# Optimization experiments

Measured on AMD Instinct MI355X. Metric: run time of the kernel, lower is better.

The kernel has to match this reference:

```python
import jax, jax.numpy as jnp
import numpy as np

N_ATOMS = 500_000
N_PAIRS = 16_000_000
A0 = 0.5291772105638411
KE = 14.399645351950548
KEHALF = KE / 2.0


def softplus_inverse(x):
    # inverse of softplus: log(exp(x) - 1)
    return float(np.log(np.expm1(x)))


def setup_inputs() -> dict:
    key = jax.random.key(0)
    k_z, k_r, k_c, k_i, k_j = jax.random.split(key, 5)
    Zf = jax.random.randint(k_z, (N_ATOMS,), 1, 95).astype(jnp.float32)
    rij = jax.random.uniform(k_r, (N_PAIRS,), minval=0.5, maxval=5.0, dtype=jnp.float32)
    cutoff_values = jax.random.uniform(k_c, (N_PAIRS,), dtype=jnp.float32)
    idx_i = jax.random.randint(k_i, (N_PAIRS,), 0, N_ATOMS)
    idx_j = jax.random.randint(k_j, (N_PAIRS,), 0, N_ATOMS)
    p = lambda v: jnp.full((1,), softplus_inverse(v), dtype=jnp.float32)
    return {
        "N": N_ATOMS,
        "Zf": Zf,
        "rij": rij,
        "cutoff_values": cutoff_values,
        "idx_i": idx_i,
        "idx_j": idx_j,
        "adiv": p(1.0 / (0.8854 * A0)),
        "apow": p(0.23),
        "c1": p(0.1818),
        "c2": p(0.5099),
        "c3": p(0.2802),
        "c4": p(0.02817),
        "a1": p(3.2),
        "a2": p(0.9423),
        "a3": p(0.4028),
        "a4": p(0.2016),
    }


def reference(N, Zf, rij, cutoff_values, idx_i, idx_j,
              adiv, apow, c1, c2, c3, c4, a1, a2, a3, a4):
    sp = jax.nn.softplus
    # per-atom screened charge: [N]
    z = Zf ** sp(apow)
    # per-pair screening length: [P]
    a = (z[idx_i] + z[idx_j]) * sp(adiv)
    a1p = sp(a1) * a
    a2p = sp(a2) * a
    a3p = sp(a3) * a
    a4p = sp(a4) * a
    c1p, c2p, c3p, c4p = sp(c1), sp(c2), sp(c3), sp(c4)
    csum = c1p + c2p + c3p + c4p
    c1n, c2n, c3n, c4n = c1p / csum, c2p / csum, c3p / csum, c4p / csum
    zizj = Zf[idx_i] * Zf[idx_j]
    f = (c1n * jnp.exp(-a1p * rij)
         + c2n * jnp.exp(-a2p * rij)
         + c3n * jnp.exp(-a3p * rij)
         + c4n * jnp.exp(-a4p * rij)) * cutoff_values
    contrib = KEHALF * f * zizj / rij  # [P]
    return jnp.zeros((N,), dtype=Zf.dtype).at[idx_i].add(contrib)
```

## Files before the change

kernel.cpp:

```cpp
#include <hip/hip_runtime.h>
#include <hip/hip_fp16.h>

static constexpr float KEHALF = 7.199822675975274f;
static constexpr int APB = 2048;
static constexpr int APB_SHIFT = 11;
static constexpr int NBMAX = 256;
static constexpr int CHUNK = 8192;
static constexpr int ABLK = 512;
static constexpr int BBLK = 1024;
static constexpr int CTILE = 1024;
static constexpr int NW_SCAN = NBMAX / 64;

typedef float v4f __attribute__((ext_vector_type(4)));
typedef int   v4i __attribute__((ext_vector_type(4)));
typedef unsigned v4u __attribute__((ext_vector_type(4)));

__global__ void zbl_tables_kernel(const float* __restrict__ adiv,
                                  const float* __restrict__ apow,
                                  const float* __restrict__ c1,
                                  const float* __restrict__ c2,
                                  const float* __restrict__ c3,
                                  const float* __restrict__ c4,
                                  const float* __restrict__ a1,
                                  const float* __restrict__ a2,
                                  const float* __restrict__ a3,
                                  const float* __restrict__ a4,
                                  float* __restrict__ consts) {
    if (threadIdx.x == 0) {
        auto sp = [](float x) { return log1pf(expf(x)); };
        float c1p = sp(*c1), c2p = sp(*c2), c3p = sp(*c3), c4p = sp(*c4);
        float inv = 1.0f / (c1p + c2p + c3p + c4p);
        consts[0] = sp(*apow);
        consts[1] = sp(*adiv);
        consts[2] = c1p * inv; consts[3] = c2p * inv;
        consts[4] = c3p * inv; consts[5] = c4p * inv;
        consts[6] = sp(*a1); consts[7] = sp(*a2);
        consts[8] = sp(*a3); consts[9] = sp(*a4);
    }
}

__global__ void zbl_pack_kernel(const float* __restrict__ Zf,
                                unsigned char* __restrict__ zb, int N) {
    int i = blockIdx.x * blockDim.x + threadIdx.x;
    if (i < N) zb[i] = (unsigned char)(Zf[i] + 0.5f);
}

__global__ void __launch_bounds__(ABLK)
zbl_phaseA(const int* __restrict__ idx_i, const int* __restrict__ idx_j,
           const float* __restrict__ rij, const float* __restrict__ cut,
           const unsigned char* __restrict__ zb,
           const float* __restrict__ consts,
           unsigned* __restrict__ recs, unsigned short* __restrict__ starts,
           int P, int NB) {
    __shared__ unsigned hist[NBMAX];
    __shared__ unsigned cursor[NBMAX];
    __shared__ unsigned wsum[NW_SCAN];

    const int t = threadIdx.x;
    const int c = blockIdx.x;
    const int base = c * CHUNK;
    const int lim = min(base + CHUNK, P);
    const int cnt = lim - base;
    const int n4 = cnt >> 2;

    for (int b = t; b < NBMAX; b += ABLK) hist[b] = 0;
    __syncthreads();

    const v4i* ii4 = reinterpret_cast<const v4i*>(idx_i + base);
    const bool p0 = t < n4;
    const bool p1 = ABLK + t < n4;
    const bool p2 = 2 * ABLK + t < n4;
    const bool p3 = 3 * ABLK + t < n4;
    v4i ii0{}, ii1{}, ii2{}, ii3{};
    if (p0) ii0 = __builtin_nontemporal_load(ii4 + t);
    if (p1) ii1 = __builtin_nontemporal_load(ii4 + ABLK + t);
    if (p2) ii2 = __builtin_nontemporal_load(ii4 + 2 * ABLK + t);
    if (p3) ii3 = __builtin_nontemporal_load(ii4 + 3 * ABLK + t);

    auto hist4 = [&](v4i ii) {
        atomicAdd(&hist[(unsigned)ii[0] >> APB_SHIFT], 1u);
        atomicAdd(&hist[(unsigned)ii[1] >> APB_SHIFT], 1u);
        atomicAdd(&hist[(unsigned)ii[2] >> APB_SHIFT], 1u);
        atomicAdd(&hist[(unsigned)ii[3] >> APB_SHIFT], 1u);
    };
    if (p0) hist4(ii0);
    if (p1) hist4(ii1);
    if (p2) hist4(ii2);
    if (p3) hist4(ii3);
    for (int p = n4 * 4 + t; p < cnt; p += ABLK)
        atomicAdd(&hist[(unsigned)idx_i[base + p] >> APB_SHIFT], 1u);
    __syncthreads();

    unsigned hv = (t < NBMAX) ? hist[t] : 0u;
    unsigned v = hv;
#pragma unroll
    for (int off = 1; off < 64; off <<= 1) {
        unsigned n = __shfl_up(v, off, 64);
        if ((t & 63) >= off) v += n;
    }
    if (t < NBMAX && (t & 63) == 63) wsum[t >> 6] = v;
    __syncthreads();
    const int S = NB + 1;
    if (t < NBMAX) {
        unsigned pre = 0;
#pragma unroll
        for (int w = 0; w < NW_SCAN - 1; ++w)
            if (w < (t >> 6)) pre += wsum[w];
        unsigned inc = v + pre;
        cursor[t] = inc - hv;
        if (t < NB)
            starts[(size_t)c * S + t + 1] = (unsigned short)inc;
    }
    if (t == 0) starts[(size_t)c * S] = 0;
    __syncthreads();

    const float sp_apow = consts[0], sp_adiv = consts[1];
    const float c1n = consts[2], c2n = consts[3], c3n = consts[4], c4n = consts[5];
    const float a1 = consts[6], a2 = consts[7], a3 = consts[8], a4 = consts[9];

    auto process = [&](int i, int j, float r, float cu) {
        unsigned bi = zb[i], bj = zb[j];
        float fi = (float)bi, fj = (float)bj;
        float zi = __expf(sp_apow * __logf(fi));
        float zj = __expf(sp_apow * __logf(fj));
        float ar = (zi + zj) * sp_adiv * r;
        float f = c1n * __expf(-a1 * ar) + c2n * __expf(-a2 * ar)
                + c3n * __expf(-a3 * ar) + c4n * __expf(-a4 * ar);
        float contrib = KEHALF * f * cu * fi * fj * __builtin_amdgcn_rcpf(r);
        unsigned b = (unsigned)i >> APB_SHIFT;
        unsigned rank = atomicAdd(&cursor[b], 1u);
        unsigned rec = (((unsigned)i & (APB - 1)) << 16)
                     | (unsigned)__half_as_ushort(__float2half_rn(contrib));
        recs[(size_t)base + rank] = rec;
    };

    const v4i* jj4 = reinterpret_cast<const v4i*>(idx_j + base);
    const v4f* rr4 = reinterpret_cast<const v4f*>(rij + base);
    const v4f* cc4 = reinterpret_cast<const v4f*>(cut + base);
    auto group = [&](v4i ii, int q) {
        v4i jj = __builtin_nontemporal_load(jj4 + q);
        v4f rr = __builtin_nontemporal_load(rr4 + q);
        v4f cc = __builtin_nontemporal_load(cc4 + q);
#pragma unroll
        for (int k = 0; k < 4; ++k) process(ii[k], jj[k], rr[k], cc[k]);
    };
    if (p0) group(ii0, t);
    if (p1) group(ii1, ABLK + t);
    if (p2) group(ii2, 2 * ABLK + t);
    if (p3) group(ii3, 3 * ABLK + t);
    for (int p = n4 * 4 + t; p < cnt; p += ABLK)
        process(idx_i[base + p], idx_j[base + p], rij[base + p], cut[base + p]);
}

__global__ void __launch_bounds__(BBLK)
zbl_phaseB(const unsigned* __restrict__ recs,
           const unsigned short* __restrict__ starts,
           float* __restrict__ out, int N, int NB, int nchunks, int cpb) {
    __shared__ float acc[APB];
    __shared__ unsigned short s0s[CTILE];
    __shared__ unsigned short s1s[CTILE];
    const int t = threadIdx.x;
    const int b = blockIdx.x;
    const int c0 = blockIdx.y * cpb;
    const int c1e = min(c0 + cpb, nchunks);
    const int S = NB + 1;
    for (int i = t; i < APB; i += BBLK) acc[i] = 0.f;

    const int hw = t >> 5, hl = t & 31, nhw = BBLK / 32;

    for (int cb = c0; cb < c1e; cb += CTILE) {
        const int ce = min(cb + CTILE, c1e);
        __syncthreads();
        for (int c = cb + t; c < ce; c += BBLK) {
            s0s[c - cb] = starts[(size_t)c * S + b];
            s1s[c - cb] = starts[(size_t)c * S + b + 1];
        }
        __syncthreads();
        for (int c = cb + hw; c < ce; c += nhw) {
            unsigned s0 = s0s[c - cb], s1 = s1s[c - cb];
            const unsigned* seg = recs + (size_t)c * CHUNK;
            for (unsigned u = s0 + hl; u < s1; u += 32) {
                unsigned rec = __builtin_nontemporal_load(seg + u);
                float v = __half2float(__ushort_as_half((unsigned short)(rec & 0xffffu)));
                atomicAdd(&acc[rec >> 16], v);
            }
        }
    }
    __syncthreads();
    const int abase = b << APB_SHIFT;
    for (int i = t; i < APB; i += BBLK) {
        int g = abase + i;
        if (g < N) atomicAdd(&out[g], acc[i]);
    }
}

__global__ void __launch_bounds__(256)
zbl_pair_fallback(const v4f* __restrict__ rij4, const v4f* __restrict__ cut4,
                  const v4i* __restrict__ ii4, const v4i* __restrict__ jj4,
                  const float* __restrict__ Zf, const float* __restrict__ consts,
                  float* __restrict__ out, int P4) {
    int t = blockIdx.x * blockDim.x + threadIdx.x;
    if (t >= P4) return;
    const float sp_apow = consts[0], sp_adiv = consts[1];
    const float c1n = consts[2], c2n = consts[3], c3n = consts[4], c4n = consts[5];
    const float a1 = consts[6], a2 = consts[7], a3 = consts[8], a4 = consts[9];
    v4f rr = rij4[t]; v4f cc = cut4[t]; v4i ii = ii4[t]; v4i jj = jj4[t];
#pragma unroll
    for (int k = 0; k < 4; ++k) {
        int i = ii[k], j = jj[k];
        float zfi = Zf[i], zfj = Zf[j];
        float zi = __expf(sp_apow * __logf(zfi));
        float zj = __expf(sp_apow * __logf(zfj));
        float a = (zi + zj) * sp_adiv;
        float ar = a * rr[k];
        float f = c1n * __expf(-a1 * ar) + c2n * __expf(-a2 * ar)
                + c3n * __expf(-a3 * ar) + c4n * __expf(-a4 * ar);
        atomicAdd(&out[i],
                  KEHALF * f * cc[k] * zfi * zfj * __builtin_amdgcn_rcpf(rr[k]));
    }
}

extern "C" void kernel_launch(void* const* d_in, const int* in_sizes, int n_in,
                              void* d_out, int out_size, void* d_ws, size_t ws_size,
                              hipStream_t stream) {
    const float* Zf = (const float*)d_in[1];
    const float* rij = (const float*)d_in[2];
    const float* cut = (const float*)d_in[3];
    const int* idx_i = (const int*)d_in[4];
    const int* idx_j = (const int*)d_in[5];
    const int N = in_sizes[1];
    const int P = in_sizes[2];
    float* out = (float*)d_out;

    const int NB = (N + APB - 1) / APB;
    const int nchunks = (P + CHUNK - 1) / CHUNK;

    size_t recs_bytes = (size_t)nchunks * CHUNK * 4;
    size_t starts_bytes = (size_t)nchunks * (NB + 1) * 2;
    size_t consts_off = (recs_bytes + starts_bytes + 255) & ~(size_t)255;
    size_t zb_off = consts_off + 16 * 4;
    size_t need = zb_off + (size_t)N + 64;

    if (NB <= NBMAX && ws_size >= need) {
        unsigned* recs = (unsigned*)d_ws;
        unsigned short* starts = (unsigned short*)((char*)d_ws + recs_bytes);
        float* consts = (float*)((char*)d_ws + consts_off);
        unsigned char* zb = (unsigned char*)((char*)d_ws + zb_off);

        zbl_tables_kernel<<<1, 64, 0, stream>>>(
            (const float*)d_in[6], (const float*)d_in[7],
            (const float*)d_in[8], (const float*)d_in[9],
            (const float*)d_in[10], (const float*)d_in[11],
            (const float*)d_in[12], (const float*)d_in[13],
            (const float*)d_in[14], (const float*)d_in[15], consts);

        zbl_pack_kernel<<<(N + 255) / 256, 256, 0, stream>>>(Zf, zb, N);

        hipMemsetAsync(out, 0, (size_t)out_size * sizeof(float), stream);

        zbl_phaseA<<<nchunks, ABLK, 0, stream>>>(
            idx_i, idx_j, rij, cut, zb, consts, recs, starts, P, NB);

        int SPLIT = (2048 + NB - 1) / NB;
        if (SPLIT < 1) SPLIT = 1;
        if (SPLIT > 16) SPLIT = 16;
        const int cpb = (nchunks + SPLIT - 1) / SPLIT;
        dim3 gridB(NB, SPLIT);
        zbl_phaseB<<<gridB, BBLK, 0, stream>>>(recs, starts, out, N, NB,
                                               nchunks, cpb);
    } else {
        float* consts = (float*)d_ws;
        hipMemsetAsync(out, 0, (size_t)out_size * sizeof(float), stream);
        zbl_tables_kernel<<<1, 64, 0, stream>>>(
            (const float*)d_in[6], (const float*)d_in[7],
            (const float*)d_in[8], (const float*)d_in[9],
            (const float*)d_in[10], (const float*)d_in[11],
            (const float*)d_in[12], (const float*)d_in[13],
            (const float*)d_in[14], (const float*)d_in[15], consts);
        zbl_pair_fallback<<<(P / 4 + 255) / 256, 256, 0, stream>>>(
            (const v4f*)rij, (const v4f*)cut, (const v4i*)idx_i,
            (const v4i*)idx_j, Zf, consts, out, P / 4);
    }
}
```

Baseline: 542.6 us.

## Stage bucketed records in LDS, transpose starts layout, prefetch idx_i Z bytes

Phase A now scatters each packed record into a 32 KB shared-memory staging buffer and writes the whole chunk to global memory with coalesced vector nontemporal stores. Previously each record was scattered straight to global memory. The starts table is transposed to bucket-major order, so phase B reads contiguous rows per bucket instead of a strided column. Z bytes for idx_i are gathered early, right after the index loads, so they overlap the histogram. The extra LDS and a barrier may lower phase A occupancy.

Result: faster. 453.7 us (-16.4%).

```diff
diff --git a/kernel.cpp b/kernel.cpp
--- a/kernel.cpp
+++ b/kernel.cpp
@@ -51,16 +51,16 @@
            const unsigned char* __restrict__ zb,
            const float* __restrict__ consts,
            unsigned* __restrict__ recs, unsigned short* __restrict__ starts,
-           int P, int NB) {
+           int P, int NB, int nchunks) {
     __shared__ unsigned hist[NBMAX];
     __shared__ unsigned cursor[NBMAX];
     __shared__ unsigned wsum[NW_SCAN];
+    __shared__ unsigned stage[CHUNK];
 
     const int t = threadIdx.x;
     const int c = blockIdx.x;
     const int base = c * CHUNK;
-    const int lim = min(base + CHUNK, P);
-    const int cnt = lim - base;
+    const int cnt = min(base + CHUNK, P) - base;
     const int n4 = cnt >> 2;
 
     for (int b = t; b < NBMAX; b += ABLK) hist[b] = 0;
@@ -76,6 +76,16 @@
     if (p1) ii1 = __builtin_nontemporal_load(ii4 + ABLK + t);
     if (p2) ii2 = __builtin_nontemporal_load(ii4 + 2 * ABLK + t);
     if (p3) ii3 = __builtin_nontemporal_load(ii4 + 3 * ABLK + t);
+
+    auto packb = [&](v4i ii) -> unsigned {
+        return (unsigned)zb[ii[0]] | ((unsigned)zb[ii[1]] << 8)
+             | ((unsigned)zb[ii[2]] << 16) | ((unsigned)zb[ii[3]] << 24);
+    };
+    unsigned bp0 = 0, bp1 = 0, bp2 = 0, bp3 = 0;
+    if (p0) bp0 = packb(ii0);
+    if (p1) bp1 = packb(ii1);
+    if (p2) bp2 = packb(ii2);
+    if (p3) bp3 = packb(ii3);
 
     auto hist4 = [&](v4i ii) {
         atomicAdd(&hist[(unsigned)ii[0] >> APB_SHIFT], 1u);
@@ -100,7 +110,6 @@
     }
     if (t < NBMAX && (t & 63) == 63) wsum[t >> 6] = v;
     __syncthreads();
-    const int S = NB + 1;
     if (t < NBMAX) {
         unsigned pre = 0;
 #pragma unroll
@@ -109,17 +118,16 @@
         unsigned inc = v + pre;
         cursor[t] = inc - hv;
         if (t < NB)
-            starts[(size_t)c * S + t + 1] = (unsigned short)inc;
-    }
-    if (t == 0) starts[(size_t)c * S] = 0;
+            starts[(size_t)(t + 1) * nchunks + c] = (unsigned short)inc;
+    }
+    if (t == 0) starts[c] = 0;
     __syncthreads();
 
     const float sp_apow = consts[0], sp_adiv = consts[1];
     const float c1n = consts[2], c2n = consts[3], c3n = consts[4], c4n = consts[5];
     const float a1 = consts[6], a2 = consts[7], a3 = consts[8], a4 = consts[9];
 
-    auto process = [&](int i, int j, float r, float cu) {
-        unsigned bi = zb[i], bj = zb[j];
+    auto process = [&](int i, unsigned bi, unsigned bj, float r, float cu) {
         float fi = (float)bi, fj = (float)bj;
         float zi = __expf(sp_apow * __logf(fi));
         float zj = __expf(sp_apow * __logf(fj));
@@ -129,27 +137,37 @@
         float contrib = KEHALF * f * cu * fi * fj * __builtin_amdgcn_rcpf(r);
         unsigned b = (unsigned)i >> APB_SHIFT;
         unsigned rank = atomicAdd(&cursor[b], 1u);
-        unsigned rec = (((unsigned)i & (APB - 1)) << 16)
-                     | (unsigned)__half_as_ushort(__float2half_rn(contrib));
-        recs[(size_t)base + rank] = rec;
+        stage[rank] = (((unsigned)i & (APB - 1)) << 16)
+                    | (unsigned)__half_as_ushort(__float2half_rn(contrib));
     };
 
     const v4i* jj4 = reinterpret_cast<const v4i*>(idx_j + base);
     const v4f* rr4 = reinterpret_cast<const v4f*>(rij + base);
     const v4f* cc4 = reinterpret_cast<const v4f*>(cut + base);
-    auto group = [&](v4i ii, int q) {
+    auto group = [&](v4i ii, unsigned bp, int q) {
         v4i jj = __builtin_nontemporal_load(jj4 + q);
         v4f rr = __builtin_nontemporal_load(rr4 + q);
         v4f cc = __builtin_nontemporal_load(cc4 + q);
 #pragma unroll
-        for (int k = 0; k < 4; ++k) process(ii[k], jj[k], rr[k], cc[k]);
+        for (int k = 0; k < 4; ++k)
+            process(ii[k], (bp >> (8 * k)) & 0xffu, zb[jj[k]], rr[k], cc[k]);
     };
-    if (p0) group(ii0, t);
-    if (p1) group(ii1, ABLK + t);
-    if (p2) group(ii2, 2 * ABLK + t);
-    if (p3) group(ii3, 3 * ABLK + t);
-    for (int p = n4 * 4 + t; p < cnt; p += ABLK)
-        process(idx_i[base + p], idx_j[base + p], rij[base + p], cut[base + p]);
+    if (p0) group(ii0, bp0, t);
+    if (p1) group(ii1, bp1, ABLK + t);
+    if (p2) group(ii2, bp2, 2 * ABLK + t);
+    if (p3) group(ii3, bp3, 3 * ABLK + t);
+    for (int p = n4 * 4 + t; p < cnt; p += ABLK) {
+        int i = idx_i[base + p];
+        process(i, zb[i], zb[idx_j[base + p]], rij[base + p], cut[base + p]);
+    }
+    __syncthreads();
+
+    {
+        const v4u* src = reinterpret_cast<const v4u*>(stage);
+        v4u* dst = reinterpret_cast<v4u*>(recs + (size_t)base);
+        for (int k = t; k < CHUNK / 4; k += ABLK)
+            __builtin_nontemporal_store(src[k], dst + k);
+    }
 }
 
 __global__ void __launch_bounds__(BBLK)
@@ -163,17 +181,18 @@
     const int b = blockIdx.x;
     const int c0 = blockIdx.y * cpb;
     const int c1e = min(c0 + cpb, nchunks);
-    const int S = NB + 1;
     for (int i = t; i < APB; i += BBLK) acc[i] = 0.f;
 
+    const unsigned short* s0row = starts + (size_t)b * nchunks;
+    const unsigned short* s1row = starts + (size_t)(b + 1) * nchunks;
     const int hw = t >> 5, hl = t & 31, nhw = BBLK / 32;
 
     for (int cb = c0; cb < c1e; cb += CTILE) {
         const int ce = min(cb + CTILE, c1e);
         __syncthreads();
         for (int c = cb + t; c < ce; c += BBLK) {
-            s0s[c - cb] = starts[(size_t)c * S + b];
-            s1s[c - cb] = starts[(size_t)c * S + b + 1];
+            s0s[c - cb] = s0row[c];
+            s1s[c - cb] = s1row[c];
         }
         __syncthreads();
         for (int c = cb + hw; c < ce; c += nhw) {
@@ -236,7 +255,7 @@
     const int nchunks = (P + CHUNK - 1) / CHUNK;
 
     size_t recs_bytes = (size_t)nchunks * CHUNK * 4;
-    size_t starts_bytes = (size_t)nchunks * (NB + 1) * 2;
+    size_t starts_bytes = (size_t)(NB + 1) * nchunks * 2;
     size_t consts_off = (recs_bytes + starts_bytes + 255) & ~(size_t)255;
     size_t zb_off = consts_off + 16 * 4;
     size_t need = zb_off + (size_t)N + 64;
@@ -259,7 +278,7 @@
         hipMemsetAsync(out, 0, (size_t)out_size * sizeof(float), stream);
 
         zbl_phaseA<<<nchunks, ABLK, 0, stream>>>(
-            idx_i, idx_j, rij, cut, zb, consts, recs, starts, P, NB);
+            idx_i, idx_j, rij, cut, zb, consts, recs, starts, P, NB, nchunks);
 
         int SPLIT = (2048 + NB - 1) / NB;
         if (SPLIT < 1) SPLIT = 1;
```
